# Performance work log

Measured on AMD Instinct MI355X. Metric: run time of the kernel, lower is better.

Reference implementation:

```python
import jax, jax.numpy as jnp
import numpy as np
from jax import lax

V, E, H, B, T = 50000, 100, 64, 128, 1024


def setup_inputs() -> dict:
    key = jax.random.key(0)
    ks = jax.random.split(key, 16)
    def u(k, shape, fan):
        s = 1.0 / np.sqrt(fan)
        return jax.random.uniform(k, shape, jnp.float32, -s, s)
    x = jax.random.randint(ks[0], (B, T), 0, V)
    emb = jax.random.normal(ks[1], (V, E), jnp.float32)
    emb = emb.at[0].set(0.0)  # padding_idx=0
    return {
        'x': x,
        'emb': emb,
        'Wih0': u(ks[2], (4 * H, E), H), 'Whh0': u(ks[3], (4 * H, H), H),
        'bih0': u(ks[4], (4 * H,), H), 'bhh0': u(ks[5], (4 * H,), H),
        'Wih1': u(ks[6], (4 * H, H), H), 'Whh1': u(ks[7], (4 * H, H), H),
        'bih1': u(ks[8], (4 * H,), H), 'bhh1': u(ks[9], (4 * H,), H),
        'W1': u(ks[10], (H, H), H), 'b1': u(ks[11], (H,), H),
        'W2': u(ks[12], (1, H), H), 'b2': u(ks[13], (1,), H),
    }


def lstm_layer(inp, Wih, Whh, bih, bhh):
    # inp: [B, T, D]; PyTorch gate order i, f, g, o
    b, h = inp.shape[0], Whh.shape[1]
    xw = jnp.einsum('btd,gd->btg', inp, Wih) + bih + bhh  # [B, T, 4H]
    def step(carry, xw_t):
        hs, cs = carry
        gates = xw_t + hs @ Whh.T
        i, f, g, o = jnp.split(gates, 4, axis=-1)
        cs = jax.nn.sigmoid(f) * cs + jax.nn.sigmoid(i) * jnp.tanh(g)
        hs = jax.nn.sigmoid(o) * jnp.tanh(cs)
        return (hs, cs), hs
    init = (jnp.zeros((b, h), inp.dtype), jnp.zeros((b, h), inp.dtype))
    _, out = lax.scan(step, init, jnp.swapaxes(xw, 0, 1))  # [T, B, H]
    return jnp.swapaxes(out, 0, 1)


def reference(x, emb, Wih0, Whh0, bih0, bhh0, Wih1, Whh1, bih1, bhh1, W1, b1, W2, b2):
    e = emb[x]                                  # [B, T, E]
    h0 = lstm_layer(e, Wih0, Whh0, bih0, bhh0)  # [B, T, H]
    h1 = lstm_layer(h0, Wih1, Whh1, bih1, bhh1) # [B, T, H]
    last = h1[:, -1, :]                         # [B, H]
    z = jax.nn.relu(last @ W1.T + b1)           # dropout is identity in eval
    return jax.nn.sigmoid(z @ W2.T + b2)        # [B, 1]
```

## Files before the change

### kernel.cpp

```cpp
#include <hip/hip_runtime.h>
#include <hip/hip_bf16.h>

#define EMB_D 100
#define HID 64
#define G4 256
#define BATCH 128
#define SEQ 1024
#define TOK 16

typedef _Float16 half2v __attribute__((ext_vector_type(2)));
typedef unsigned short u16;
typedef unsigned int   u32;

__device__ __forceinline__ float rcpf(float x) { return __builtin_amdgcn_rcpf(x); }
__device__ __forceinline__ float sigf(float x) {
  return rcpf(1.0f + __expf(-x));
}
__device__ __forceinline__ float tanh_fast(float x) {
  float t = __expf(-2.0f * fabsf(x));
  float r = (1.0f - t) * rcpf(1.0f + t);
  return copysignf(r, x);
}

__device__ __forceinline__ float dot2(u32 h, u32 w, float acc) {
  return __builtin_amdgcn_fdot2(__builtin_bit_cast(half2v, h),
                                __builtin_bit_cast(half2v, w), acc, false);
}

__device__ __forceinline__ u32 packh2(float lo, float hi) {
  u16 a = __builtin_bit_cast(u16, (_Float16)lo);
  u16 b = __builtin_bit_cast(u16, (_Float16)hi);
  return (u32)a | ((u32)b << 16);
}

#define QP_XOR1 0xB1
#define QP_XOR2 0x4E
#define QP_XOR3 0x1B
#define QPERM(x, ctrl)                                                        \
  __builtin_bit_cast(float, __builtin_amdgcn_mov_dpp(                         \
      __builtin_bit_cast(int, (x)), (ctrl), 0xF, 0xF, true))

__global__ void prep_kernel(const float* __restrict__ Wih0,
                            const float* __restrict__ Whh0, const float* __restrict__ Wih1,
                            const float* __restrict__ Whh1,
                            const float* __restrict__ bih0, const float* __restrict__ bhh0,
                            const float* __restrict__ bih1, const float* __restrict__ bhh1,
                            float* __restrict__ Wih0T, float* __restrict__ b0c,
                            float* __restrict__ b1c,
                            u32* __restrict__ Whh0h, u32* __restrict__ Wih1h,
                            u32* __restrict__ Whh1h) {
  int g = threadIdx.x;
  b0c[g] = bih0[g] + bhh0[g];
  b1c[g] = bih1[g] + bhh1[g];
  for (int d = 0; d < EMB_D; ++d) Wih0T[d * G4 + g] = Wih0[g * EMB_D + d];
  for (int d = 0; d < HID / 2; ++d) {
    Whh0h[g * 32 + d] = packh2(Whh0[g * HID + 2 * d], Whh0[g * HID + 2 * d + 1]);
    Wih1h[g * 32 + d] = packh2(Wih1[g * HID + 2 * d], Wih1[g * HID + 2 * d + 1]);
    Whh1h[g * 32 + d] = packh2(Whh1[g * HID + 2 * d], Whh1[g * HID + 2 * d + 1]);
  }
}

__global__ __attribute__((amdgpu_waves_per_eu(1, 4))) __launch_bounds__(256)
void xw0_kernel(
    const int* __restrict__ x, const float* __restrict__ emb,
    const float* __restrict__ Wih0T, const float* __restrict__ b0c,
    _Float16* __restrict__ xw0h) {
  __shared__ int sidx[TOK];
  __shared__ float erow[TOK][EMB_D];
  int g = threadIdx.x;
  long t0 = (long)blockIdx.x * TOK;

  if (g < TOK) sidx[g] = x[t0 + g];
  __syncthreads();
  for (int i = g; i < TOK * 25; i += 256) {
    int tok = i / 25;
    int d4 = i - tok * 25;
    const float4 v = *(const float4*)(emb + (size_t)sidx[tok] * EMB_D + 4 * d4);
    erow[tok][4 * d4]     = v.x;
    erow[tok][4 * d4 + 1] = v.y;
    erow[tok][4 * d4 + 2] = v.z;
    erow[tok][4 * d4 + 3] = v.w;
  }

  float w[EMB_D];
  #pragma unroll
  for (int d = 0; d < EMB_D; ++d) w[d] = Wih0T[d * G4 + g];
  float bb = b0c[g];
  __syncthreads();

  for (int tok = 0; tok < TOK; ++tok) {
    const float* ev = erow[tok];
    float a0 = bb, a1 = 0.f, a2 = 0.f, a3 = 0.f;
    #pragma unroll
    for (int d = 0; d < EMB_D; d += 4) {
      a0 = fmaf(w[d],     ev[d],     a0);
      a1 = fmaf(w[d + 1], ev[d + 1], a1);
      a2 = fmaf(w[d + 2], ev[d + 2], a2);
      a3 = fmaf(w[d + 3], ev[d + 3], a3);
    }
    xw0h[(t0 + tok) * G4 + g] = (_Float16)((a0 + a1) + (a2 + a3));
  }
}

__global__ __launch_bounds__(512, 2) void lstm_fused_kernel(
    const _Float16* __restrict__ xw0h,
    const u32* __restrict__ Whh0h, const u32* __restrict__ Wih1h,
    const u32* __restrict__ Whh1h, const float* __restrict__ b1c,
    const float* __restrict__ W1, const float* __restrict__ clsb1,
    const float* __restrict__ W2, const float* __restrict__ clsb2,
    float* __restrict__ out) {
  int tid = threadIdx.x;
  int lane = tid & 63;
  int w = tid >> 6;
  bool isL1 = (w >= 4);
  int eg = isL1 ? (w - 4) : w;
  int e = eg * 16 + (lane >> 2);
  int k = lane & 3;
  int row = k * HID + e;
  int b = blockIdx.x;

  __shared__ alignas(16) _Float16 h0s[2][HID];
  __shared__ alignas(16) _Float16 h1s[2][HID];
  __shared__ alignas(16) float hf[HID];

  uint4 wA[8], wB[8];
  if (!isL1) {
    const uint4* p = (const uint4*)(Whh0h + row * 32);
    #pragma unroll
    for (int c = 0; c < 8; ++c) wA[c] = p[c];
  } else {
    const uint4* p = (const uint4*)(Wih1h + row * 32);
    const uint4* q = (const uint4*)(Whh1h + row * 32);
    #pragma unroll
    for (int c = 0; c < 8; ++c) { wA[c] = p[c]; wB[c] = q[c]; }
  }
  float bias = isL1 ? b1c[row] : 0.f;

  if (tid < 2 * HID) {
    int j = tid & (HID - 1);
    if (tid < HID) { h0s[0][j] = (_Float16)0.f; h0s[1][j] = (_Float16)0.f; }
    else           { h1s[0][j] = (_Float16)0.f; h1s[1][j] = (_Float16)0.f; }
  }

  const _Float16* xr = xw0h + (long)b * SEQ * G4 + row;
  float xw_t = 0.f, xw_t1 = 0.f;
  if (!isL1) { xw_t = (float)xr[0]; xw_t1 = (float)xr[G4]; }
  float c_reg = 0.f;
  __syncthreads();

  for (int t = 0; t < SEQ; ++t) {
    float xw_t2 = 0.f;
    if (!isL1) {
      int tn = (t + 2 < SEQ) ? (t + 2) : (SEQ - 1);
      xw_t2 = (float)xr[(long)tn * G4];
    }
    int rb = (t + 1) & 1, wbuf = t & 1;
    const uint4* h0p = (const uint4*)h0s[rb];
    float gown;
    if (!isL1) {
      float a0 = xw_t, a1 = 0.f, a2 = 0.f, a3 = 0.f;
      #pragma unroll
      for (int c = 0; c < 8; ++c) {
        uint4 h = h0p[c];
        a0 = dot2(h.x, wA[c].x, a0);
        a1 = dot2(h.y, wA[c].y, a1);
        a2 = dot2(h.z, wA[c].z, a2);
        a3 = dot2(h.w, wA[c].w, a3);
      }
      gown = (a0 + a1) + (a2 + a3);
    } else {
      const uint4* h1p = (const uint4*)h1s[rb];
      float a0 = bias, a1 = 0.f, a2 = 0.f, a3 = 0.f;
      float b0 = 0.f, b1 = 0.f, b2 = 0.f, b3 = 0.f;
      #pragma unroll
      for (int c = 0; c < 8; ++c) {
        uint4 h = h0p[c];
        uint4 g2 = h1p[c];
        a0 = dot2(h.x, wA[c].x, a0);
        a1 = dot2(h.y, wA[c].y, a1);
        a2 = dot2(h.z, wA[c].z, a2);
        a3 = dot2(h.w, wA[c].w, a3);
        b0 = dot2(g2.x, wB[c].x, b0);
        b1 = dot2(g2.y, wB[c].y, b1);
        b2 = dot2(g2.z, wB[c].z, b2);
        b3 = dot2(g2.w, wB[c].w, b3);
      }
      gown = ((a0 + a1) + (a2 + a3)) + ((b0 + b1) + (b2 + b3));
    }
    float gx1 = QPERM(gown, QP_XOR1);
    float gx2 = QPERM(gown, QP_XOR2);
    float gx3 = QPERM(gown, QP_XOR3);
    bool act = (!isL1) || (t > 0);
    if (act) {
      c_reg = sigf(gx1) * c_reg + sigf(gown) * tanh_fast(gx2);
      float hv = sigf(gx3) * tanh_fast(c_reg);
      if (k == 0) {
        _Float16 h16 = (_Float16)hv;
        if (isL1) h1s[wbuf][e] = h16; else h0s[wbuf][e] = h16;
      }
    }
    xw_t = xw_t1; xw_t1 = xw_t2;
    asm volatile("s_waitcnt lgkmcnt(0)" ::: "memory");
    __builtin_amdgcn_s_barrier();
    asm volatile("" ::: "memory");
  }

  if (isL1) {
    const uint4* h0p = (const uint4*)h0s[1];
    const uint4* h1p = (const uint4*)h1s[1];
    float a0 = bias, a1 = 0.f, a2 = 0.f, a3 = 0.f;
    float b0 = 0.f, b1 = 0.f, b2 = 0.f, b3 = 0.f;
    #pragma unroll
    for (int c = 0; c < 8; ++c) {
      uint4 h = h0p[c];
      uint4 g2 = h1p[c];
      a0 = dot2(h.x, wA[c].x, a0);
      a1 = dot2(h.y, wA[c].y, a1);
      a2 = dot2(h.z, wA[c].z, a2);
      a3 = dot2(h.w, wA[c].w, a3);
      b0 = dot2(g2.x, wB[c].x, b0);
      b1 = dot2(g2.y, wB[c].y, b1);
      b2 = dot2(g2.z, wB[c].z, b2);
      b3 = dot2(g2.w, wB[c].w, b3);
    }
    float gown = ((a0 + a1) + (a2 + a3)) + ((b0 + b1) + (b2 + b3));
    float gx1 = QPERM(gown, QP_XOR1);
    float gx2 = QPERM(gown, QP_XOR2);
    float gx3 = QPERM(gown, QP_XOR3);
    c_reg = sigf(gx1) * c_reg + sigf(gown) * tanh_fast(gx2);
    float hv = sigf(gx3) * tanh_fast(c_reg);
    if (k == 0) hf[e] = hv;
  }
  __syncthreads();

  if (w == 0) {
    int j = lane;
    const float4* wp = (const float4*)(W1 + j * HID);
    const float4* hp = (const float4*)hf;
    float z0 = clsb1[j], z1 = 0.f, z2 = 0.f, z3 = 0.f;
    #pragma unroll
    for (int c = 0; c < 16; ++c) {
      float4 wv = wp[c];
      float4 hv = hp[c];
      z0 = fmaf(hv.x, wv.x, z0);
      z1 = fmaf(hv.y, wv.y, z1);
      z2 = fmaf(hv.z, wv.z, z2);
      z3 = fmaf(hv.w, wv.w, z3);
    }
    float z = fmaxf((z0 + z1) + (z2 + z3), 0.f);
    float v = z * W2[j];
    v += __shfl_xor(v, 1);
    v += __shfl_xor(v, 2);
    v += __shfl_xor(v, 4);
    v += __shfl_xor(v, 8);
    v += __shfl_xor(v, 16);
    v += __shfl_xor(v, 32);
    if (lane == 0) out[b] = sigf(v + clsb2[0]);
  }
}

extern "C" void kernel_launch(void* const* d_in, const int* in_sizes, int n_in,
                              void* d_out, int out_size, void* d_ws, size_t ws_size,
                              hipStream_t stream) {
  const int*   x    = (const int*)d_in[0];
  const float* emb  = (const float*)d_in[1];
  const float* Wih0 = (const float*)d_in[2];
  const float* Whh0 = (const float*)d_in[3];
  const float* bih0 = (const float*)d_in[4];
  const float* bhh0 = (const float*)d_in[5];
  const float* Wih1 = (const float*)d_in[6];
  const float* Whh1 = (const float*)d_in[7];
  const float* bih1 = (const float*)d_in[8];
  const float* bhh1 = (const float*)d_in[9];
  const float* W1   = (const float*)d_in[10];
  const float* b1   = (const float*)d_in[11];
  const float* W2   = (const float*)d_in[12];
  const float* b2   = (const float*)d_in[13];
  float* out = (float*)d_out;

  char* ws = (char*)d_ws;
  const size_t XW0_BYTES = (size_t)BATCH * SEQ * G4 * sizeof(_Float16);
  _Float16* xw0h = (_Float16*)ws;                 ws += XW0_BYTES;
  float* Wih0T   = (float*)ws;                    ws += (size_t)EMB_D * G4 * sizeof(float);
  float* b0c     = (float*)ws;                    ws += G4 * sizeof(float);
  float* b1c     = (float*)ws;                    ws += G4 * sizeof(float);
  u32* Whh0h     = (u32*)ws;                      ws += (size_t)G4 * 32 * sizeof(u32);
  u32* Wih1h     = (u32*)ws;                      ws += (size_t)G4 * 32 * sizeof(u32);
  u32* Whh1h     = (u32*)ws;                      ws += (size_t)G4 * 32 * sizeof(u32);

  prep_kernel<<<1, 256, 0, stream>>>(Wih0, Whh0, Wih1, Whh1, bih0, bhh0, bih1, bhh1,
                                     Wih0T, b0c, b1c, Whh0h, Wih1h, Whh1h);
  xw0_kernel<<<(BATCH * SEQ) / TOK, 256, 0, stream>>>(x, emb, Wih0T, b0c, xw0h);
  lstm_fused_kernel<<<BATCH, 512, 0, stream>>>(xw0h, Whh0h, Wih1h, Whh1h, b1c,
                                               W1, b1, W2, b2, out);
}
```

Before: 882.0 us.

## Split layer-1 input projection across waves and move embedding projection to fp16 dot2

Layer-0 waves now also compute half of the layer-1 input projection (Wih1 times h0) from the h0 values they already loaded, and pass the partial sums to layer-1 waves through shared memory. This is meant to balance per-step dot-product work between the two wave groups. The extra stage needs a third h0 buffer and two extra loop iterations. The xw0 kernel now packs embeddings and Wih0 to fp16 and uses dot2 with 64 tokens per block, which lowers precision of the input projection.

```diff
diff --git a/kernel.cpp b/kernel.cpp
--- a/kernel.cpp
+++ b/kernel.cpp
@@ -6,33 +6,28 @@
 #define G4 256
 #define BATCH 128
 #define SEQ 1024
-#define TOK 16
+#define TOK 64
 
 typedef _Float16 half2v __attribute__((ext_vector_type(2)));
 typedef unsigned short u16;
 typedef unsigned int   u32;
 
 __device__ __forceinline__ float rcpf(float x) { return __builtin_amdgcn_rcpf(x); }
-__device__ __forceinline__ float sigf(float x) {
-  return rcpf(1.0f + __expf(-x));
-}
+__device__ __forceinline__ float sigf(float x) { return rcpf(1.0f + __expf(-x)); }
 __device__ __forceinline__ float tanh_fast(float x) {
   float t = __expf(-2.0f * fabsf(x));
   float r = (1.0f - t) * rcpf(1.0f + t);
   return copysignf(r, x);
 }
-
 __device__ __forceinline__ float dot2(u32 h, u32 w, float acc) {
   return __builtin_amdgcn_fdot2(__builtin_bit_cast(half2v, h),
                                 __builtin_bit_cast(half2v, w), acc, false);
 }
-
 __device__ __forceinline__ u32 packh2(float lo, float hi) {
   u16 a = __builtin_bit_cast(u16, (_Float16)lo);
   u16 b = __builtin_bit_cast(u16, (_Float16)hi);
   return (u32)a | ((u32)b << 16);
 }
-
 #define QP_XOR1 0xB1
 #define QP_XOR2 0x4E
 #define QP_XOR3 0x1B
@@ -45,15 +40,16 @@
                             const float* __restrict__ Whh1,
                             const float* __restrict__ bih0, const float* __restrict__ bhh0,
                             const float* __restrict__ bih1, const float* __restrict__ bhh1,
-                            float* __restrict__ Wih0T, float* __restrict__ b0c,
+                            u32* __restrict__ Wih0T2, float* __restrict__ b0c,
                             float* __restrict__ b1c,
                             u32* __restrict__ Whh0h, u32* __restrict__ Wih1h,
                             u32* __restrict__ Whh1h) {
   int g = threadIdx.x;
   b0c[g] = bih0[g] + bhh0[g];
   b1c[g] = bih1[g] + bhh1[g];
-  for (int d = 0; d < EMB_D; ++d) Wih0T[d * G4 + g] = Wih0[g * EMB_D + d];
-  for (int d = 0; d < HID / 2; ++d) {
+  for (int dp = 0; dp < 50; ++dp)
+    Wih0T2[dp * G4 + g] = packh2(Wih0[g * EMB_D + 2 * dp], Wih0[g * EMB_D + 2 * dp + 1]);
+  for (int d = 0; d < 32; ++d) {
     Whh0h[g * 32 + d] = packh2(Whh0[g * HID + 2 * d], Whh0[g * HID + 2 * d + 1]);
     Wih1h[g * 32 + d] = packh2(Wih1[g * HID + 2 * d], Wih1[g * HID + 2 * d + 1]);
     Whh1h[g * 32 + d] = packh2(Whh1[g * HID + 2 * d], Whh1[g * HID + 2 * d + 1]);
@@ -63,40 +59,39 @@
 __global__ __attribute__((amdgpu_waves_per_eu(1, 4))) __launch_bounds__(256)
 void xw0_kernel(
     const int* __restrict__ x, const float* __restrict__ emb,
-    const float* __restrict__ Wih0T, const float* __restrict__ b0c,
+    const u32* __restrict__ Wih0T2, const float* __restrict__ b0c,
     _Float16* __restrict__ xw0h) {
   __shared__ int sidx[TOK];
-  __shared__ float erow[TOK][EMB_D];
+  __shared__ alignas(16) u32 erow[TOK][52];
   int g = threadIdx.x;
   long t0 = (long)blockIdx.x * TOK;
 
   if (g < TOK) sidx[g] = x[t0 + g];
   __syncthreads();
-  for (int i = g; i < TOK * 25; i += 256) {
-    int tok = i / 25;
-    int d4 = i - tok * 25;
-    const float4 v = *(const float4*)(emb + (size_t)sidx[tok] * EMB_D + 4 * d4);
-    erow[tok][4 * d4]     = v.x;
-    erow[tok][4 * d4 + 1] = v.y;
-    erow[tok][4 * d4 + 2] = v.z;
-    erow[tok][4 * d4 + 3] = v.w;
-  }
-
-  float w[EMB_D];
+  for (int i = g; i < TOK * 50; i += 256) {
+    int tok = i / 50, dp = i - tok * 50;
+    const float* er = emb + (size_t)sidx[tok] * EMB_D + 2 * dp;
+    erow[tok][dp] = packh2(er[0], er[1]);
+  }
+  for (int i = g; i < TOK * 2; i += 256) erow[i >> 1][50 + (i & 1)] = 0;
+
+  u32 wreg[52];
   #pragma unroll
-  for (int d = 0; d < EMB_D; ++d) w[d] = Wih0T[d * G4 + g];
+  for (int dp = 0; dp < 50; ++dp) wreg[dp] = Wih0T2[dp * G4 + g];
+  wreg[50] = 0; wreg[51] = 0;
   float bb = b0c[g];
   __syncthreads();
 
   for (int tok = 0; tok < TOK; ++tok) {
-    const float* ev = erow[tok];
+    const uint4* ep = (const uint4*)erow[tok];
     float a0 = bb, a1 = 0.f, a2 = 0.f, a3 = 0.f;
     #pragma unroll
-    for (int d = 0; d < EMB_D; d += 4) {
-      a0 = fmaf(w[d],     ev[d],     a0);
-      a1 = fmaf(w[d + 1], ev[d + 1], a1);
-      a2 = fmaf(w[d + 2], ev[d + 2], a2);
-      a3 = fmaf(w[d + 3], ev[d + 3], a3);
+    for (int c = 0; c < 13; ++c) {
+      uint4 hv = ep[c];
+      a0 = dot2(hv.x, wreg[4 * c],     a0);
+      a1 = dot2(hv.y, wreg[4 * c + 1], a1);
+      a2 = dot2(hv.z, wreg[4 * c + 2], a2);
+      a3 = dot2(hv.w, wreg[4 * c + 3], a3);
     }
     xw0h[(t0 + tok) * G4 + g] = (_Float16)((a0 + a1) + (a2 + a3));
   }
@@ -119,28 +114,31 @@
   int row = k * HID + e;
   int b = blockIdx.x;
 
-  __shared__ alignas(16) _Float16 h0s[2][HID];
+  __shared__ alignas(16) _Float16 h0s[3][HID];
   __shared__ alignas(16) _Float16 h1s[2][HID];
+  __shared__ float ps[2][4][65];
   __shared__ alignas(16) float hf[HID];
 
-  uint4 wA[8], wB[8];
+  uint4 wA[8], wP[4];
   if (!isL1) {
     const uint4* p = (const uint4*)(Whh0h + row * 32);
     #pragma unroll
     for (int c = 0; c < 8; ++c) wA[c] = p[c];
+    const uint4* q = (const uint4*)(Wih1h + row * 32);
+    #pragma unroll
+    for (int c = 0; c < 4; ++c) wP[c] = q[c];
   } else {
-    const uint4* p = (const uint4*)(Wih1h + row * 32);
-    const uint4* q = (const uint4*)(Whh1h + row * 32);
-    #pragma unroll
-    for (int c = 0; c < 8; ++c) { wA[c] = p[c]; wB[c] = q[c]; }
+    const uint4* q = (const uint4*)(Wih1h + row * 32);
+    #pragma unroll
+    for (int c = 0; c < 4; ++c) wP[c] = q[4 + c];
+    const uint4* p = (const uint4*)(Whh1h + row * 32);
+    #pragma unroll
+    for (int c = 0; c < 8; ++c) wA[c] = p[c];
   }
   float bias = isL1 ? b1c[row] : 0.f;
 
-  if (tid < 2 * HID) {
-    int j = tid & (HID - 1);
-    if (tid < HID) { h0s[0][j] = (_Float16)0.f; h0s[1][j] = (_Float16)0.f; }
-    else           { h1s[0][j] = (_Float16)0.f; h1s[1][j] = (_Float16)0.f; }
-  }
+  if (tid < 3 * HID) ((u16*)h0s)[tid] = 0;
+  if (tid < 2 * HID) ((u16*)h1s)[tid] = 0;
 
   const _Float16* xr = xw0h + (long)b * SEQ * G4 + row;
   float xw_t = 0.f, xw_t1 = 0.f;
@@ -148,90 +146,89 @@
   float c_reg = 0.f;
   __syncthreads();
 
-  for (int t = 0; t < SEQ; ++t) {
-    float xw_t2 = 0.f;
+  int h0w = 0, h0rA = 2, h0rB = 1;
+  for (int t = 0; t <= SEQ + 1; ++t) {
     if (!isL1) {
-      int tn = (t + 2 < SEQ) ? (t + 2) : (SEQ - 1);
-      xw_t2 = (float)xr[(long)tn * G4];
-    }
-    int rb = (t + 1) & 1, wbuf = t & 1;
-    const uint4* h0p = (const uint4*)h0s[rb];
-    float gown;
-    if (!isL1) {
-      float a0 = xw_t, a1 = 0.f, a2 = 0.f, a3 = 0.f;
-      #pragma unroll
-      for (int c = 0; c < 8; ++c) {
-        uint4 h = h0p[c];
-        a0 = dot2(h.x, wA[c].x, a0);
-        a1 = dot2(h.y, wA[c].y, a1);
-        a2 = dot2(h.z, wA[c].z, a2);
-        a3 = dot2(h.w, wA[c].w, a3);
+      if (t <= SEQ) {
+        const uint4* h0p = (const uint4*)h0s[h0rA];
+        uint4 hc[8];
+        #pragma unroll
+        for (int c = 0; c < 8; ++c) hc[c] = h0p[c];
+        {
+          float p0 = 0.f, p1 = 0.f, p2 = 0.f, p3 = 0.f;
+          #pragma unroll
+          for (int c = 0; c < 4; ++c) {
+            p0 = dot2(hc[c].x, wP[c].x, p0);
+            p1 = dot2(hc[c].y, wP[c].y, p1);
+            p2 = dot2(hc[c].z, wP[c].z, p2);
+            p3 = dot2(hc[c].w, wP[c].w, p3);
+          }
+          ps[t & 1][k][e] = (p0 + p1) + (p2 + p3);
+        }
+        if (t < SEQ) {
+          float a0 = xw_t, a1 = 0.f, a2 = 0.f, a3 = 0.f;
+          #pragma unroll
+          for (int c = 0; c < 8; ++c) {
+            a0 = dot2(hc[c].x, wA[c].x, a0);
+            a1 = dot2(hc[c].y, wA[c].y, a1);
+            a2 = dot2(hc[c].z, wA[c].z, a2);
+            a3 = dot2(hc[c].w, wA[c].w, a3);
+          }
+          float gown = (a0 + a1) + (a2 + a3);
+          float gx1 = QPERM(gown, QP_XOR1);
+          float gx2 = QPERM(gown, QP_XOR2);
+          float gx3 = QPERM(gown, QP_XOR3);
+          c_reg = sigf(gx1) * c_reg + sigf(gown) * tanh_fast(gx2);
+          float hv = sigf(gx3) * tanh_fast(c_reg);
+          if (k == 0) h0s[h0w][e] = (_Float16)hv;
+          float xw_t2 = 0.f;
+          int tn = (t + 2 < SEQ) ? (t + 2) : (SEQ - 1);
+          xw_t2 = (float)xr[(long)tn * G4];
+          xw_t = xw_t1; xw_t1 = xw_t2;
+        }
       }
-      gown = (a0 + a1) + (a2 + a3);
     } else {
-      const uint4* h1p = (const uint4*)h1s[rb];
-      float a0 = bias, a1 = 0.f, a2 = 0.f, a3 = 0.f;
-      float b0 = 0.f, b1 = 0.f, b2 = 0.f, b3 = 0.f;
-      #pragma unroll
-      for (int c = 0; c < 8; ++c) {
-        uint4 h = h0p[c];
-        uint4 g2 = h1p[c];
-        a0 = dot2(h.x, wA[c].x, a0);
-        a1 = dot2(h.y, wA[c].y, a1);
-        a2 = dot2(h.z, wA[c].z, a2);
-        a3 = dot2(h.w, wA[c].w, a3);
-        b0 = dot2(g2.x, wB[c].x, b0);
-        b1 = dot2(g2.y, wB[c].y, b1);
-        b2 = dot2(g2.z, wB[c].z, b2);
-        b3 = dot2(g2.w, wB[c].w, b3);
-      }
-      gown = ((a0 + a1) + (a2 + a3)) + ((b0 + b1) + (b2 + b3));
-    }
-    float gx1 = QPERM(gown, QP_XOR1);
-    float gx2 = QPERM(gown, QP_XOR2);
-    float gx3 = QPERM(gown, QP_XOR3);
-    bool act = (!isL1) || (t > 0);
-    if (act) {
-      c_reg = sigf(gx1) * c_reg + sigf(gown) * tanh_fast(gx2);
-      float hv = sigf(gx3) * tanh_fast(c_reg);
-      if (k == 0) {
-        _Float16 h16 = (_Float16)hv;
-        if (isL1) h1s[wbuf][e] = h16; else h0s[wbuf][e] = h16;
+      if (t >= 2) {
+        const uint4* h0p = (const uint4*)h0s[h0rB];
+        const uint4* h1p = (const uint4*)h1s[(t + 1) & 1];
+        float a0 = bias, a1 = 0.f, a2 = 0.f, a3 = 0.f;
+        float b0 = 0.f, b1 = 0.f, b2 = 0.f, b3 = 0.f;
+        #pragma unroll
+        for (int c = 0; c < 4; ++c) {
+          uint4 h = h0p[4 + c];
+          a0 = dot2(h.x, wP[c].x, a0);
+          a1 = dot2(h.y, wP[c].y, a1);
+          a2 = dot2(h.z, wP[c].z, a2);
+          a3 = dot2(h.w, wP[c].w, a3);
+        }
+        #pragma unroll
+        for (int c = 0; c < 8; ++c) {
+          uint4 h = h1p[c];
+          b0 = dot2(h.x, wA[c].x, b0);
+          b1 = dot2(h.y, wA[c].y, b1);
+          b2 = dot2(h.z, wA[c].z, b2);
+          b3 = dot2(h.w, wA[c].w, b3);
+        }
+        float gown = ((a0 + a1) + (a2 + a3)) + ((b0 + b1) + (b2 + b3))
+                     + ps[(t + 1) & 1][k][e];
+        float gx1 = QPERM(gown, QP_XOR1);
+        float gx2 = QPERM(gown, QP_XOR2);
+        float gx3 = QPERM(gown, QP_XOR3);
+        c_reg = sigf(gx1) * c_reg + sigf(gown) * tanh_fast(gx2);
+        float hv = sigf(gx3) * tanh_fast(c_reg);
+        if (k == 0) {
+          h1s[t & 1][e] = (_Float16)hv;
+          if (t == SEQ + 1) hf[e] = hv;
+        }
       }
     }
-    xw_t = xw_t1; xw_t1 = xw_t2;
+    h0w = (h0w == 2) ? 0 : h0w + 1;
+    h0rA = (h0rA == 2) ? 0 : h0rA + 1;
+    h0rB = (h0rB == 2) ? 0 : h0rB + 1;
     asm volatile("s_waitcnt lgkmcnt(0)" ::: "memory");
     __builtin_amdgcn_s_barrier();
     asm volatile("" ::: "memory");
   }
-
-  if (isL1) {
-    const uint4* h0p = (const uint4*)h0s[1];
-    const uint4* h1p = (const uint4*)h1s[1];
-    float a0 = bias, a1 = 0.f, a2 = 0.f, a3 = 0.f;
-    float b0 = 0.f, b1 = 0.f, b2 = 0.f, b3 = 0.f;
-    #pragma unroll
-    for (int c = 0; c < 8; ++c) {
-      uint4 h = h0p[c];
-      uint4 g2 = h1p[c];
-      a0 = dot2(h.x, wA[c].x, a0);
-      a1 = dot2(h.y, wA[c].y, a1);
-      a2 = dot2(h.z, wA[c].z, a2);
-      a3 = dot2(h.w, wA[c].w, a3);
-      b0 = dot2(g2.x, wB[c].x, b0);
-      b1 = dot2(g2.y, wB[c].y, b1);
-      b2 = dot2(g2.z, wB[c].z, b2);
-      b3 = dot2(g2.w, wB[c].w, b3);
-    }
-    float gown = ((a0 + a1) + (a2 + a3)) + ((b0 + b1) + (b2 + b3));
-    float gx1 = QPERM(gown, QP_XOR1);
-    float gx2 = QPERM(gown, QP_XOR2);
-    float gx3 = QPERM(gown, QP_XOR3);
-    c_reg = sigf(gx1) * c_reg + sigf(gown) * tanh_fast(gx2);
-    float hv = sigf(gx3) * tanh_fast(c_reg);
-    if (k == 0) hf[e] = hv;
-  }
-  __syncthreads();
 
   if (w == 0) {
     int j = lane;
@@ -280,17 +277,17 @@
 
   char* ws = (char*)d_ws;
   const size_t XW0_BYTES = (size_t)BATCH * SEQ * G4 * sizeof(_Float16);
-  _Float16* xw0h = (_Float16*)ws;                 ws += XW0_BYTES;
-  float* Wih0T   = (float*)ws;                    ws += (size_t)EMB_D * G4 * sizeof(float);
-  float* b0c     = (float*)ws;                    ws += G4 * sizeof(float);
-  float* b1c     = (float*)ws;                    ws += G4 * sizeof(float);
-  u32* Whh0h     = (u32*)ws;                      ws += (size_t)G4 * 32 * sizeof(u32);
-  u32* Wih1h     = (u32*)ws;                      ws += (size_t)G4 * 32 * sizeof(u32);
-  u32* Whh1h     = (u32*)ws;                      ws += (size_t)G4 * 32 * sizeof(u32);
+  _Float16* xw0h = (_Float16*)ws;     ws += XW0_BYTES;
+  u32* Wih0T2    = (u32*)ws;          ws += (size_t)50 * G4 * sizeof(u32);
+  float* b0c     = (float*)ws;        ws += G4 * sizeof(float);
+  float* b1c     = (float*)ws;        ws += G4 * sizeof(float);
+  u32* Whh0h     = (u32*)ws;          ws += (size_t)G4 * 32 * sizeof(u32);
+  u32* Wih1h     = (u32*)ws;          ws += (size_t)G4 * 32 * sizeof(u32);
+  u32* Whh1h     = (u32*)ws;          ws += (size_t)G4 * 32 * sizeof(u32);
 
   prep_kernel<<<1, 256, 0, stream>>>(Wih0, Whh0, Wih1, Whh1, bih0, bhh0, bih1, bhh1,
-                                     Wih0T, b0c, b1c, Whh0h, Wih1h, Whh1h);
-  xw0_kernel<<<(BATCH * SEQ) / TOK, 256, 0, stream>>>(x, emb, Wih0T, b0c, xw0h);
+                                     Wih0T2, b0c, b1c, Whh0h, Wih1h, Whh1h);
+  xw0_kernel<<<(BATCH * SEQ) / TOK, 256, 0, stream>>>(x, emb, Wih0T2, b0c, xw0h);
   lstm_fused_kernel<<<BATCH, 512, 0, stream>>>(xw0h, Whh0h, Wih1h, Whh1h, b1c,
                                                W1, b1, W2, b2, out);
 }
```

After: 782.8 us. 11.2% less time.
